# Kernel optimization log

Hardware: AMD Instinct MI355X
Metric: run time of the kernel (lower is better)

The kernel has to match this reference:

```python
import jax, jax.numpy as jnp
import numpy as np

N_NODES = 100000
N_EDGES = 1600000
N_GRAPHS = 5000
NODE_DIM = 16
EDGE_DIM = 16
HID = 20


def setup_inputs() -> dict:
    key = jax.random.key(0)
    ks = jax.random.split(key, 12)
    edge_index = jax.random.randint(ks[0], (2, N_EDGES), 0, N_NODES)
    node_attr = jax.random.normal(ks[1], (N_NODES, NODE_DIM), dtype=jnp.float32)
    edge_attr = jax.random.normal(ks[2], (N_EDGES, EDGE_DIM), dtype=jnp.float32)
    batch = jnp.sort(jax.random.randint(ks[3], (N_NODES,), 0, N_GRAPHS))
    s = 0.1
    W_msg = jax.random.normal(ks[4], (2 * NODE_DIM + EDGE_DIM, HID), dtype=jnp.float32) * s
    b_msg = jnp.zeros((HID,), dtype=jnp.float32)
    W1 = jax.random.normal(ks[5], (HID, 10), dtype=jnp.float32) * s
    b1 = jnp.zeros((10,), dtype=jnp.float32)
    W2 = jax.random.normal(ks[6], (10, 10), dtype=jnp.float32) * s
    b2 = jnp.zeros((10,), dtype=jnp.float32)
    W3 = jax.random.normal(ks[7], (10, 1), dtype=jnp.float32) * s
    b3 = jnp.zeros((1,), dtype=jnp.float32)
    return {"edge_index": edge_index, "node_attr": node_attr, "edge_attr": edge_attr,
            "batch": batch, "W_msg": W_msg, "b_msg": b_msg, "W1": W1, "b1": b1,
            "W2": W2, "b2": b2, "W3": W3, "b3": b3}


def reference(edge_index, node_attr, edge_attr, batch,
              W_msg, b_msg, W1, b1, W2, b2, W3, b3):
    src, dst = edge_index[0], edge_index[1]
    # MPL_1: gather -> linear -> relu -> scatter-sum to destination nodes
    feats = jnp.concatenate([node_attr[src], node_attr[dst], edge_attr], axis=-1)  # [E, 48]
    msg = jax.nn.relu(feats @ W_msg + b_msg)  # [E, 20]
    x = jax.ops.segment_sum(msg, dst, num_segments=N_NODES)  # [N, 20]
    # node MLP + graph pooling (segment_coo sum over batch) + graph MLP
    x = jax.nn.relu(x @ W1 + b1)  # [N, 10]
    g = jax.ops.segment_sum(x, batch, num_segments=N_GRAPHS)  # [G, 10]
    g = jax.nn.relu(g @ W2 + b2)
    return g @ W3 + b3  # [G, 1]
```

## Files before the change

### kernel.cpp

```cpp
#include <hip/hip_runtime.h>

constexpr int NN = 100000;
constexpr int NE = 1600000;
constexpr int NG = 5000;
constexpr int BKT = 64;
constexpr int NBKT = (NN + BKT - 1) / BKT;
constexpr int NB = 128;
constexpr int CHUNK = NE / NB;

constexpr size_t OFF_G  = 2000000;
constexpr size_t OFF_BH = OFF_G + 50000;
constexpr size_t OFF_ST = OFF_BH + (size_t)NB * NBKT;
constexpr size_t OFF_PM = OFF_ST + NBKT + 1;

__global__ __launch_bounds__(256) void k_hist(const int* __restrict__ ei,
                                              int* __restrict__ bh,
                                              float* __restrict__ g) {
  __shared__ int lh[NBKT];
  for (int i = threadIdx.x; i < NBKT; i += 256) lh[i] = 0;
  __syncthreads();
  const int* dstp = ei + NE;
  int s = blockIdx.x * CHUNK;
  for (int i = s + threadIdx.x; i < s + CHUNK; i += 256)
    atomicAdd(&lh[dstp[i] >> 6], 1);
  int gid = blockIdx.x * 256 + threadIdx.x;
  if (gid < 12500) ((float4*)g)[gid] = make_float4(0.f, 0.f, 0.f, 0.f);
  __syncthreads();
  int* out = bh + (size_t)blockIdx.x * NBKT;
  for (int k = threadIdx.x; k < NBKT; k += 256) out[k] = lh[k];
}

__global__ __launch_bounds__(256) void k_btot(const int* __restrict__ bh,
                                              int* __restrict__ starts) {
  int k = blockIdx.x * 256 + threadIdx.x;
  if (k >= NBKT) return;
  int tot = 0;
  for (int b = 0; b < NB; b += 4) {
    int a0 = bh[(size_t)(b    ) * NBKT + k];
    int a1 = bh[(size_t)(b + 1) * NBKT + k];
    int a2 = bh[(size_t)(b + 2) * NBKT + k];
    int a3 = bh[(size_t)(b + 3) * NBKT + k];
    tot += a0 + a1 + a2 + a3;
  }
  starts[k] = tot;
}

__global__ __launch_bounds__(1024) void k_sscan(int* __restrict__ starts) {
  __shared__ int s0[1024], s1[1024];
  int t = threadIdx.x;
  int k0 = 2 * t, k1 = 2 * t + 1;
  int tot0 = (k0 < NBKT) ? starts[k0] : 0;
  int tot1 = (k1 < NBKT) ? starts[k1] : 0;
  int ssum = tot0 + tot1;
  int* cur = s0; int* nxt = s1;
  cur[t] = ssum;
  __syncthreads();
  for (int off = 1; off < 1024; off <<= 1) {
    int v = cur[t];
    if (t >= off) v += cur[t - off];
    nxt[t] = v;
    __syncthreads();
    int* tmp = cur; cur = nxt; nxt = tmp;
  }
  int excl = cur[t] - ssum;
  if (k0 < NBKT) starts[k0] = excl;
  if (k1 <= NBKT) starts[k1] = excl + tot0;
}

__global__ __launch_bounds__(256) void k_bases(int* __restrict__ bh,
                                               const int* __restrict__ starts) {
  int k = blockIdx.x * 256 + threadIdx.x;
  if (k >= NBKT) return;
  int run = starts[k];
  for (int b = 0; b < NB; ++b) {
    size_t idx = (size_t)b * NBKT + k;
    int v = bh[idx];
    bh[idx] = run;
    run += v;
  }
}

__global__ __launch_bounds__(256) void k_scatter(const int* __restrict__ ei,
                                                 const int* __restrict__ bh,
                                                 int* __restrict__ perm) {
  __shared__ int base[NBKT];
  __shared__ int cnt[NBKT];
  const int* row = bh + (size_t)blockIdx.x * NBKT;
  for (int k = threadIdx.x; k < NBKT; k += 256) { base[k] = row[k]; cnt[k] = 0; }
  __syncthreads();
  const int* dstp = ei + NE;
  int s = blockIdx.x * CHUNK;
  for (int i = s + threadIdx.x; i < s + CHUNK; i += 256) {
    int d = dstp[i];
    int k = d >> 6;
    int r = atomicAdd(&cnt[k], 1);
    perm[base[k] + r] = i | ((d & 63) << 24);
  }
}

#define ST4(A, B, V) { A[B] = (V).x; A[B+1] = (V).y; A[B+2] = (V).z; A[B+3] = (V).w; }

__global__ __launch_bounds__(256, 2) void k_edge(
    const int* __restrict__ ei,
    const float* __restrict__ nattr,
    const float* __restrict__ eattr,
    const float* __restrict__ Wm,
    const float* __restrict__ bm,
    const int* __restrict__ perm,
    const int* __restrict__ starts,
    float* __restrict__ x) {
  __shared__ float xt[20 * 65];
  __shared__ int s_se[2];
  for (int i = threadIdx.x; i < 20 * 65; i += 256) xt[i] = 0.f;
  if (threadIdx.x < 2) s_se[threadIdx.x] = starts[blockIdx.x + threadIdx.x];
  __syncthreads();
  int is = s_se[0], ie = s_se[1];
  int nbase = blockIdx.x * BKT;

  int wave = threadIdx.x >> 6;
  int lane = threadIdx.x & 63;
  int ep = lane / 10;
  int jp = lane - ep * 10;
  bool act = ep < 6;
  int epc = act ? ep : 0;

  float W0[48], W1[48];
#pragma unroll
  for (int k = 0; k < 48; ++k) {
    W0[k] = Wm[k * 20 + 2 * jp];
    W1[k] = Wm[k * 20 + 2 * jp + 1];
  }
#pragma unroll
  for (int k = 0; k < 48; ++k) {
    asm volatile("" : "+v"(W0[k]));
    asm volatile("" : "+v"(W1[k]));
  }
  float bj0 = bm[2 * jp], bj1 = bm[2 * jp + 1];

  int base = is + wave * 6;
  int iC = base + epc;
  int pC = 0, sC = 0;
  if (base < ie) {
    pC = perm[min(iC, ie - 1)];
    sC = ei[pC & 0xFFFFFF];
  }
  while (base < ie) {
    int baseN = base + 24;
    int iN = baseN + epc;
    int pN = 0, sN = 0;
    if (baseN < ie) {
      pN = perm[min(iN, ie - 1)];
      sN = ei[pN & 0xFFFFFF];
    }

    int e  = pC & 0xFFFFFF;
    int dl = (pC >> 24) & 63;
    const float4* ps = (const float4*)(nattr + (size_t)sC * 16);
    const float4* pd = (const float4*)(nattr + (size_t)(nbase + dl) * 16);
    const float4* pe = (const float4*)(eattr + (size_t)e * 16);

    float f[48];
    { float4 t0 = ps[0], t1 = ps[1], t2 = ps[2], t3 = ps[3];
      ST4(f, 0, t0) ST4(f, 4, t1) ST4(f, 8, t2) ST4(f, 12, t3) }
    { float4 t0 = pd[0], t1 = pd[1], t2 = pd[2], t3 = pd[3];
      ST4(f, 16, t0) ST4(f, 20, t1) ST4(f, 24, t2) ST4(f, 28, t3) }
    { float4 t0 = pe[0], t1 = pe[1], t2 = pe[2], t3 = pe[3];
      ST4(f, 32, t0) ST4(f, 36, t1) ST4(f, 40, t2) ST4(f, 44, t3) }
#pragma unroll
    for (int k = 0; k < 48; ++k) asm volatile("" : "+v"(f[k]));

    float a0 = bj0, a1 = bj1;
#pragma unroll
    for (int k = 0; k < 48; ++k) {
      a0 = fmaf(f[k], W0[k], a0);
      a1 = fmaf(f[k], W1[k], a1);
    }

    bool valid = act && (iC < ie);
    float m0 = fmaxf(a0, 0.f);
    float m1 = fmaxf(a1, 0.f);
    if (valid && m0 > 0.f) atomicAdd(&xt[(2 * jp) * 65 + dl], m0);
    if (valid && m1 > 0.f) atomicAdd(&xt[(2 * jp + 1) * 65 + dl], m1);

    base = baseN; iC = iN; pC = pN; sC = sN;
  }
  __syncthreads();

  int nn = min(BKT, NN - nbase);
  float* xo = x + (size_t)nbase * 20;
  for (int idx = threadIdx.x; idx < nn * 20; idx += 256) {
    int node = idx / 20;
    int j = idx - node * 20;
    xo[idx] = xt[j * 65 + node];
  }
}

constexpr int SPAN = 512;
__global__ __launch_bounds__(256) void k_node(
    const float* __restrict__ x,
    const int* __restrict__ batch,
    const float* __restrict__ W1,
    const float* __restrict__ b1,
    float* __restrict__ g) {
  __shared__ float gacc[SPAN * 10];
  __shared__ int s_bmin;
  for (int i = threadIdx.x; i < SPAN * 10; i += 256) gacc[i] = 0.f;
  int n0 = blockIdx.x * 256;
  if (threadIdx.x == 0) s_bmin = batch[n0];
  __syncthreads();
  int bmin = s_bmin;
  int n = n0 + threadIdx.x;
  if (n < NN) {
    float xi[20];
    const float4* px = (const float4*)(x + (size_t)n * 20);
    { float4 t0 = px[0], t1 = px[1], t2 = px[2], t3 = px[3], t4 = px[4];
      ST4(xi, 0, t0) ST4(xi, 4, t1) ST4(xi, 8, t2) ST4(xi, 12, t3) ST4(xi, 16, t4) }
    float acc[10];
#pragma unroll
    for (int j = 0; j < 10; ++j) acc[j] = b1[j];
#pragma unroll
    for (int k = 0; k < 20; ++k) {
      float fk = xi[k];
#pragma unroll
      for (int j = 0; j < 10; ++j) acc[j] = fmaf(fk, W1[k * 10 + j], acc[j]);
    }
    int bn = batch[n];
    int d = bn - bmin;
    if (d < SPAN) {
#pragma unroll
      for (int j = 0; j < 10; ++j) {
        float m = fmaxf(acc[j], 0.f);
        if (m > 0.f) atomicAdd(&gacc[d * 10 + j], m);
      }
    } else {
#pragma unroll
      for (int j = 0; j < 10; ++j) {
        float m = fmaxf(acc[j], 0.f);
        if (m > 0.f) unsafeAtomicAdd(&g[(size_t)bn * 10 + j], m);
      }
    }
  }
  __syncthreads();
  int lim = min(SPAN * 10, NG * 10 - bmin * 10);
  float* gp = g + (size_t)bmin * 10;
  for (int idx = threadIdx.x; idx < lim; idx += 256) {
    float v = gacc[idx];
    if (v != 0.f) unsafeAtomicAdd(&gp[idx], v);
  }
}

__global__ __launch_bounds__(256) void k_graph(
    const float* __restrict__ g,
    const float* __restrict__ W2, const float* __restrict__ b2,
    const float* __restrict__ W3, const float* __restrict__ b3,
    float* __restrict__ out) {
  int i = blockIdx.x * 256 + threadIdx.x;
  if (i >= NG) return;
  float gi[10];
  const float2* pg = (const float2*)(g + (size_t)i * 10);
#pragma unroll
  for (int k = 0; k < 5; ++k) { float2 v = pg[k]; gi[2*k] = v.x; gi[2*k+1] = v.y; }
  float o = b3[0];
#pragma unroll
  for (int j = 0; j < 10; ++j) {
    float a = b2[j];
#pragma unroll
    for (int k = 0; k < 10; ++k) a = fmaf(gi[k], W2[k * 10 + j], a);
    o = fmaf(fmaxf(a, 0.f), W3[j], o);
  }
  out[i] = o;
}

extern "C" void kernel_launch(void* const* d_in, const int* in_sizes, int n_in,
                              void* d_out, int out_size, void* d_ws, size_t ws_size,
                              hipStream_t stream) {
  const int*   ei    = (const int*)  d_in[0];
  const float* nattr = (const float*)d_in[1];
  const float* eattr = (const float*)d_in[2];
  const int*   batch = (const int*)  d_in[3];
  const float* Wm    = (const float*)d_in[4];
  const float* bm    = (const float*)d_in[5];
  const float* W1    = (const float*)d_in[6];
  const float* b1    = (const float*)d_in[7];
  const float* W2    = (const float*)d_in[8];
  const float* b2    = (const float*)d_in[9];
  const float* W3    = (const float*)d_in[10];
  const float* b3    = (const float*)d_in[11];

  float* x      = (float*)d_ws;
  float* g      = (float*)d_ws + OFF_G;
  int*   bh     = (int*)d_ws + OFF_BH;
  int*   starts = (int*)d_ws + OFF_ST;
  int*   perm   = (int*)d_ws + OFF_PM;

  constexpr int SCAN_BLKS = (NBKT + 255) / 256;

  k_hist   <<<NB, 256, 0, stream>>>(ei, bh, g);
  k_btot   <<<SCAN_BLKS, 256, 0, stream>>>(bh, starts);
  k_sscan  <<<1, 1024, 0, stream>>>(starts);
  k_bases  <<<SCAN_BLKS, 256, 0, stream>>>(bh, starts);
  k_scatter<<<NB, 256, 0, stream>>>(ei, bh, perm);
  k_edge   <<<NBKT, 256, 0, stream>>>(ei, nattr, eattr, Wm, bm, perm, starts, x);
  k_node   <<<(NN + 255) / 256, 256, 0, stream>>>(x, batch, W1, b1, g);
  k_graph  <<<(NG + 255) / 256, 256, 0, stream>>>(g, W2, b2, W3, b3, (float*)d_out);
}
```

Before: 442.0 us.

## Fuse node MLP and graph pooling into edge kernel, use packed FMA, prefetch gathers

The node MLP and per-graph pooling now run in the epilogue of the edge kernel, reading the per-bucket node sums straight from shared memory. This drops the x buffer round trip through global memory and one kernel launch. The edge dot product now uses 2-wide vector FMAs with four partial accumulators, and the next edge's source-node and edge-attribute rows are loaded one iteration ahead. The costs are extra live registers for the prefetched float4s and an epilogue where only 64 of 256 threads do work.

```diff
diff --git a/kernel.cpp b/kernel.cpp
--- a/kernel.cpp
+++ b/kernel.cpp
@@ -8,8 +8,10 @@
 constexpr int NB = 128;
 constexpr int CHUNK = NE / NB;
 
-constexpr size_t OFF_G  = 2000000;
-constexpr size_t OFF_BH = OFF_G + 50000;
+typedef float v2f __attribute__((ext_vector_type(2)));
+
+constexpr size_t OFF_G  = 0;
+constexpr size_t OFF_BH = 50048;
 constexpr size_t OFF_ST = OFF_BH + (size_t)NB * NBKT;
 constexpr size_t OFF_PM = OFF_ST + NBKT + 1;
 
@@ -98,7 +100,11 @@
   }
 }
 
-#define ST4(A, B, V) { A[B] = (V).x; A[B+1] = (V).y; A[B+2] = (V).z; A[B+3] = (V).w; }
+#define PK4(V, K0) \
+  a0 = __builtin_elementwise_fma(v2f{(V).x, (V).x}, W[K0+0], a0); \
+  a1 = __builtin_elementwise_fma(v2f{(V).y, (V).y}, W[K0+1], a1); \
+  a2 = __builtin_elementwise_fma(v2f{(V).z, (V).z}, W[K0+2], a2); \
+  a3 = __builtin_elementwise_fma(v2f{(V).w, (V).w}, W[K0+3], a3);
 
 __global__ __launch_bounds__(256, 2) void k_edge(
     const int* __restrict__ ei,
@@ -106,16 +112,23 @@
     const float* __restrict__ eattr,
     const float* __restrict__ Wm,
     const float* __restrict__ bm,
+    const int* __restrict__ batch,
+    const float* __restrict__ W1,
+    const float* __restrict__ b1,
     const int* __restrict__ perm,
     const int* __restrict__ starts,
-    float* __restrict__ x) {
+    float* __restrict__ g) {
   __shared__ float xt[20 * 65];
+  __shared__ float gb[64 * 10];
   __shared__ int s_se[2];
+  __shared__ int s_bmin;
   for (int i = threadIdx.x; i < 20 * 65; i += 256) xt[i] = 0.f;
+  for (int i = threadIdx.x; i < 640; i += 256) gb[i] = 0.f;
   if (threadIdx.x < 2) s_se[threadIdx.x] = starts[blockIdx.x + threadIdx.x];
+  int nbase = blockIdx.x * BKT;
+  if (threadIdx.x == 0) s_bmin = batch[nbase];
   __syncthreads();
   int is = s_se[0], ie = s_se[1];
-  int nbase = blockIdx.x * BKT;
 
   int wave = threadIdx.x >> 6;
   int lane = threadIdx.x & 63;
@@ -124,25 +137,25 @@
   bool act = ep < 6;
   int epc = act ? ep : 0;
 
-  float W0[48], W1[48];
-#pragma unroll
-  for (int k = 0; k < 48; ++k) {
-    W0[k] = Wm[k * 20 + 2 * jp];
-    W1[k] = Wm[k * 20 + 2 * jp + 1];
-  }
-#pragma unroll
-  for (int k = 0; k < 48; ++k) {
-    asm volatile("" : "+v"(W0[k]));
-    asm volatile("" : "+v"(W1[k]));
-  }
-  float bj0 = bm[2 * jp], bj1 = bm[2 * jp + 1];
+  v2f W[48];
+#pragma unroll
+  for (int k = 0; k < 48; ++k)
+    W[k] = v2f{Wm[k * 20 + 2 * jp], Wm[k * 20 + 2 * jp + 1]};
+#pragma unroll
+  for (int k = 0; k < 48; ++k) asm volatile("" : "+v"(W[k]));
+  v2f bj = {bm[2 * jp], bm[2 * jp + 1]};
 
   int base = is + wave * 6;
   int iC = base + epc;
   int pC = 0, sC = 0;
+  float4 e0, e1, e2, e3, n0, n1, n2, n3;
   if (base < ie) {
     pC = perm[min(iC, ie - 1)];
     sC = ei[pC & 0xFFFFFF];
+    const float4* pe = (const float4*)(eattr + (size_t)(pC & 0xFFFFFF) * 16);
+    const float4* ps = (const float4*)(nattr + (size_t)sC * 16);
+    e0 = pe[0]; e1 = pe[1]; e2 = pe[2]; e3 = pe[3];
+    n0 = ps[0]; n1 = ps[1]; n2 = ps[2]; n3 = ps[3];
   }
   while (base < ie) {
     int baseN = base + 24;
@@ -152,69 +165,40 @@
       pN = perm[min(iN, ie - 1)];
       sN = ei[pN & 0xFFFFFF];
     }
-
-    int e  = pC & 0xFFFFFF;
+    const float4* peN = (const float4*)(eattr + (size_t)(pN & 0xFFFFFF) * 16);
+    const float4* psN = (const float4*)(nattr + (size_t)sN * 16);
+    float4 e0N = peN[0], e1N = peN[1], e2N = peN[2], e3N = peN[3];
+    float4 n0N = psN[0], n1N = psN[1], n2N = psN[2], n3N = psN[3];
+
     int dl = (pC >> 24) & 63;
-    const float4* ps = (const float4*)(nattr + (size_t)sC * 16);
     const float4* pd = (const float4*)(nattr + (size_t)(nbase + dl) * 16);
-    const float4* pe = (const float4*)(eattr + (size_t)e * 16);
-
-    float f[48];
-    { float4 t0 = ps[0], t1 = ps[1], t2 = ps[2], t3 = ps[3];
-      ST4(f, 0, t0) ST4(f, 4, t1) ST4(f, 8, t2) ST4(f, 12, t3) }
-    { float4 t0 = pd[0], t1 = pd[1], t2 = pd[2], t3 = pd[3];
-      ST4(f, 16, t0) ST4(f, 20, t1) ST4(f, 24, t2) ST4(f, 28, t3) }
-    { float4 t0 = pe[0], t1 = pe[1], t2 = pe[2], t3 = pe[3];
-      ST4(f, 32, t0) ST4(f, 36, t1) ST4(f, 40, t2) ST4(f, 44, t3) }
-#pragma unroll
-    for (int k = 0; k < 48; ++k) asm volatile("" : "+v"(f[k]));
-
-    float a0 = bj0, a1 = bj1;
-#pragma unroll
-    for (int k = 0; k < 48; ++k) {
-      a0 = fmaf(f[k], W0[k], a0);
-      a1 = fmaf(f[k], W1[k], a1);
-    }
+    float4 u0 = pd[0], u1 = pd[1], u2 = pd[2], u3 = pd[3];
+
+    v2f a0 = {0.f, 0.f}, a1 = {0.f, 0.f}, a2 = {0.f, 0.f}, a3 = {0.f, 0.f};
+    PK4(n0, 0)  PK4(n1, 4)  PK4(n2, 8)  PK4(n3, 12)
+    PK4(u0, 16) PK4(u1, 20) PK4(u2, 24) PK4(u3, 28)
+    PK4(e0, 32) PK4(e1, 36) PK4(e2, 40) PK4(e3, 44)
+    v2f r = ((a0 + a1) + (a2 + a3)) + bj;
 
     bool valid = act && (iC < ie);
-    float m0 = fmaxf(a0, 0.f);
-    float m1 = fmaxf(a1, 0.f);
+    float m0 = fmaxf(r.x, 0.f);
+    float m1 = fmaxf(r.y, 0.f);
     if (valid && m0 > 0.f) atomicAdd(&xt[(2 * jp) * 65 + dl], m0);
     if (valid && m1 > 0.f) atomicAdd(&xt[(2 * jp + 1) * 65 + dl], m1);
 
     base = baseN; iC = iN; pC = pN; sC = sN;
+    e0 = e0N; e1 = e1N; e2 = e2N; e3 = e3N;
+    n0 = n0N; n1 = n1N; n2 = n2N; n3 = n3N;
   }
   __syncthreads();
 
   int nn = min(BKT, NN - nbase);
-  float* xo = x + (size_t)nbase * 20;
-  for (int idx = threadIdx.x; idx < nn * 20; idx += 256) {
-    int node = idx / 20;
-    int j = idx - node * 20;
-    xo[idx] = xt[j * 65 + node];
-  }
-}
-
-constexpr int SPAN = 512;
-__global__ __launch_bounds__(256) void k_node(
-    const float* __restrict__ x,
-    const int* __restrict__ batch,
-    const float* __restrict__ W1,
-    const float* __restrict__ b1,
-    float* __restrict__ g) {
-  __shared__ float gacc[SPAN * 10];
-  __shared__ int s_bmin;
-  for (int i = threadIdx.x; i < SPAN * 10; i += 256) gacc[i] = 0.f;
-  int n0 = blockIdx.x * 256;
-  if (threadIdx.x == 0) s_bmin = batch[n0];
-  __syncthreads();
   int bmin = s_bmin;
-  int n = n0 + threadIdx.x;
-  if (n < NN) {
+  if (threadIdx.x < 64 && (int)threadIdx.x < nn) {
+    int node = threadIdx.x;
     float xi[20];
-    const float4* px = (const float4*)(x + (size_t)n * 20);
-    { float4 t0 = px[0], t1 = px[1], t2 = px[2], t3 = px[3], t4 = px[4];
-      ST4(xi, 0, t0) ST4(xi, 4, t1) ST4(xi, 8, t2) ST4(xi, 12, t3) ST4(xi, 16, t4) }
+#pragma unroll
+    for (int j = 0; j < 20; ++j) xi[j] = xt[j * 65 + node];
     float acc[10];
 #pragma unroll
     for (int j = 0; j < 10; ++j) acc[j] = b1[j];
@@ -224,13 +208,13 @@
 #pragma unroll
       for (int j = 0; j < 10; ++j) acc[j] = fmaf(fk, W1[k * 10 + j], acc[j]);
     }
-    int bn = batch[n];
+    int bn = batch[nbase + node];
     int d = bn - bmin;
-    if (d < SPAN) {
+    if (d < 64) {
 #pragma unroll
       for (int j = 0; j < 10; ++j) {
         float m = fmaxf(acc[j], 0.f);
-        if (m > 0.f) atomicAdd(&gacc[d * 10 + j], m);
+        if (m > 0.f) atomicAdd(&gb[d * 10 + j], m);
       }
     } else {
 #pragma unroll
@@ -241,10 +225,10 @@
     }
   }
   __syncthreads();
-  int lim = min(SPAN * 10, NG * 10 - bmin * 10);
+  int glim = min(640, NG * 10 - bmin * 10);
   float* gp = g + (size_t)bmin * 10;
-  for (int idx = threadIdx.x; idx < lim; idx += 256) {
-    float v = gacc[idx];
+  for (int idx = threadIdx.x; idx < glim; idx += 256) {
+    float v = gb[idx];
     if (v != 0.f) unsafeAtomicAdd(&gp[idx], v);
   }
 }
@@ -287,7 +271,6 @@
   const float* W3    = (const float*)d_in[10];
   const float* b3    = (const float*)d_in[11];
 
-  float* x      = (float*)d_ws;
   float* g      = (float*)d_ws + OFF_G;
   int*   bh     = (int*)d_ws + OFF_BH;
   int*   starts = (int*)d_ws + OFF_ST;
@@ -300,7 +283,7 @@
   k_sscan  <<<1, 1024, 0, stream>>>(starts);
   k_bases  <<<SCAN_BLKS, 256, 0, stream>>>(bh, starts);
   k_scatter<<<NB, 256, 0, stream>>>(ei, bh, perm);
-  k_edge   <<<NBKT, 256, 0, stream>>>(ei, nattr, eattr, Wm, bm, perm, starts, x);
-  k_node   <<<(NN + 255) / 256, 256, 0, stream>>>(x, batch, W1, b1, g);
+  k_edge   <<<NBKT, 256, 0, stream>>>(ei, nattr, eattr, Wm, bm, batch, W1, b1,
+                                      perm, starts, g);
   k_graph  <<<(NG + 255) / 256, 256, 0, stream>>>(g, W2, b2, W3, b3, (float*)d_out);
 }
```

After: 439.7 us. No clear change (-0.5%).
